# Optimization experiments

Measured on AMD Instinct MI355X. Metric: run time of the kernel, lower is better.

The kernel has to match this reference:

```python
import jax, jax.numpy as jnp
import numpy as np
import math

DIM = 256
HEADS = 8
HID = DIM * HEADS


def mish(x):
    return x * jnp.tanh(jax.nn.softplus(x))


def setup_inputs() -> dict:
    key = jax.random.key(0)
    ks = jax.random.split(key, 12)
    b, t, l = 4, 16, 256
    s = 1.0 / math.sqrt(DIM)
    inp = {
        "qkv_x": jax.random.normal(ks[0], (b, t, l, DIM), jnp.float32),
        "t_embed": jax.random.normal(ks[1], (b, t, 1, DIM), jnp.float32),
        "reward_embed": jax.random.normal(ks[2], (b, t, 1, DIM), jnp.float32),
        "Wq": jax.random.normal(ks[3], (DIM, HID), jnp.float32) * s,
        "Wk": jax.random.normal(ks[4], (DIM, HID), jnp.float32) * s,
        "Wv": jax.random.normal(ks[5], (DIM, HID), jnp.float32) * s,
        "Wq_t": jax.random.normal(ks[6], (DIM, HID), jnp.float32) * s,
        "bq_t": jnp.zeros((HID,), jnp.float32),
        "Wk_t": jax.random.normal(ks[7], (DIM, HID), jnp.float32) * s,
        "bk_t": jnp.zeros((HID,), jnp.float32),
        "Wv_t": jax.random.normal(ks[8], (DIM, HID), jnp.float32) * s,
        "bv_t": jnp.zeros((HID,), jnp.float32),
        "Wo": jax.random.normal(ks[9], (HID, DIM), jnp.float32) * (1.0 / math.sqrt(HID)),
        "bo": jnp.zeros((DIM,), jnp.float32),
    }
    return inp


def reference(qkv_x, t_embed, reward_embed, Wq, Wk, Wv, Wq_t, bq_t, Wk_t, bk_t, Wv_t, bv_t, Wo, bo):
    b, t, l, f = qkv_x.shape
    x = qkv_x.reshape(b * t, l, f)                    # (bt, l, f)
    tr = (t_embed + reward_embed).reshape(b * t, 1, f)  # (bt, 1, f)
    m = mish(tr)

    def proj(W, Wt, bt_):
        # bias-add of time-conditioning broadcast over l, split heads
        y = x @ W + (m @ Wt + bt_)                    # (bt, l, H*D)
        return y.reshape(b * t, l, HEADS, DIM).transpose(0, 2, 1, 3)  # (bt, H, l, D)

    q = proj(Wq, Wq_t, bq_t)
    k = proj(Wk, Wk_t, bk_t)
    v = proj(Wv, Wv_t, bv_t)

    scores = jnp.einsum('bhqd,bhkd->bhqk', q, k) / math.sqrt(DIM)
    attn = jax.nn.softmax(scores, axis=-1)
    out = jnp.einsum('bhqk,bhkd->bhqd', attn, v)      # (bt, H, l, D)
    out = out.transpose(0, 2, 1, 3).reshape(b, t, l, HEADS * DIM)
    return out @ Wo + bo
```

## Files before the change

### kernel.cpp

```cpp
#include <hip/hip_runtime.h>
#include <stdint.h>

typedef __bf16 bf16x8 __attribute__((ext_vector_type(8)));
typedef float f32x4 __attribute__((ext_vector_type(4)));
typedef uint32_t u32x4 __attribute__((ext_vector_type(4)));

#define MFMA16(a,b,c) __builtin_amdgcn_mfma_f32_16x16x32_bf16(a,b,c,0,0,0)

#define OFF_XB   0ull
#define OFF_WT   8388608ull
#define OFF_WTT  11534336ull
#define OFF_WOT  14680064ull
#define OFF_MB   15728640ull
#define OFF_BIAS 15761408ull
#define OFF_K    17334272ull
#define OFF_VT   84443136ull
#define WS_NEED  151552000ull
#define OFF_Q    151552000ull
#define WS_NEED2 218660864ull

__device__ __forceinline__ uint16_t f2bf(float f) {
  uint32_t u = __builtin_bit_cast(uint32_t, f);
  return (uint16_t)((u + 0x7fffu + ((u >> 16) & 1u)) >> 16);
}
__device__ __forceinline__ bf16x8 ld16(const uint16_t* p) {
  u32x4 v = *(const u32x4*)p;
  return __builtin_bit_cast(bf16x8, v);
}
__device__ __forceinline__ void bounce_w2(char* slab, int row, int col, uint16_t val) {
  int slot = col >> 3;
  *(uint16_t*)(slab + row * 256 + (((slot ^ (row & 7)) & 15) << 4) + ((col & 7) << 1)) = val;
}
__device__ __forceinline__ bf16x8 bounce_r16(const char* slab, int row, int slot) {
  u32x4 v = *(const u32x4*)(slab + row * 256 + (((slot ^ (row & 7)) & 15) << 4));
  return __builtin_bit_cast(bf16x8, v);
}

__global__ void sentinel_kernel(float* out, float val) {
  out[blockIdx.x * 256 + threadIdx.x] = val;
}
__global__ void init_out(const float* bo, float* out) {
  int i = blockIdx.x * 256 + threadIdx.x;
  out[i] = bo[i & 255];
}

__global__ void mish_kernel(const float* te, const float* re, uint16_t* mb) {
  int i = blockIdx.x * 256 + threadIdx.x;
  float x = te[i] + re[i];
  float sp = log1pf(__expf(x));
  mb[i] = f2bf(x * tanhf(sp));
}

__global__ void convx_kernel(const float* x, uint16_t* xb) {
  int i = blockIdx.x * 256 + threadIdx.x;
  float4 v = ((const float4*)x)[i];
  ushort4 o = make_ushort4(f2bf(v.x), f2bf(v.y), f2bf(v.z), f2bf(v.w));
  ((ushort4*)xb)[i] = o;
}

__global__ void wtrans_kernel(const float* w0, const float* w1, const float* w2,
                              const float* w3, const float* w4, const float* w5,
                              const float* w6, uint16_t* wt, uint16_t* wtt, uint16_t* wot) {
  int z = blockIdx.y;
  const float* src; uint16_t* dst; int C;
  if (z < 3)      { src = (z==0)?w0:((z==1)?w1:w2); dst = wt  + (size_t)z*524288;     C=2048; }
  else if (z < 6) { src = (z==3)?w3:((z==4)?w4:w5); dst = wtt + (size_t)(z-3)*524288; C=2048; }
  else            { src = w6; dst = wot;                                              C=256; }
  int R = (z < 6) ? 256 : 2048;
  __shared__ uint16_t tile[32][33];
  int tc = C >> 5;
  int bR = (blockIdx.x / tc) << 5, bC = (blockIdx.x % tc) << 5;
  int tx = threadIdx.x & 31, ty = threadIdx.x >> 5;
  #pragma unroll
  for (int i = 0; i < 4; i++) {
    int r = bR + ty + i * 8;
    tile[ty + i * 8][tx] = f2bf(src[(size_t)r * C + bC + tx]);
  }
  __syncthreads();
  #pragma unroll
  for (int i = 0; i < 4; i++) {
    int c = bC + ty + i * 8;
    dst[(size_t)c * R + bR + tx] = tile[tx][ty + i * 8];
  }
}

__global__ __launch_bounds__(256, 4)
void bias_gemm(const uint16_t* Mb, const uint16_t* WTT,
               const float* bq, const float* bk, const float* bv, float* biasAll) {
  int bid = blockIdx.x;
  int z = bid >> 4, nbt = bid & 15;
  int n0 = nbt << 7;
  const uint16_t* Bsrc = WTT + (size_t)z * 524288;
  const float* bvec = (z == 0) ? bq : ((z == 1) ? bk : bv);
  float* outp = biasAll + (size_t)z * 131072;
  int tid = threadIdx.x, lane = tid & 63, w = tid >> 6;
  int g = lane >> 4, ln = lane & 15;

  bf16x8 af[8];
  #pragma unroll
  for (int ks = 0; ks < 8; ks++)
    af[ks] = ld16(Mb + (size_t)(w*16 + ln) * 256 + ks*32 + g*8);
  f32x4 acc[8];
  #pragma unroll
  for (int j = 0; j < 8; j++) acc[j] = (f32x4){0.f,0.f,0.f,0.f};
  #pragma unroll
  for (int j = 0; j < 8; j++)
    #pragma unroll
    for (int ks = 0; ks < 8; ks++) {
      bf16x8 bf_ = ld16(Bsrc + (size_t)(n0 + j*16 + ln) * 256 + ks*32 + g*8);
      acc[j] = MFMA16(af[ks], bf_, acc[j]);
    }
  #pragma unroll
  for (int j = 0; j < 8; j++) {
    int colg = n0 + j*16 + ln;
    float bb = bvec[colg];
    #pragma unroll
    for (int r = 0; r < 4; r++)
      outp[(size_t)(w*16 + g*4 + r) * 2048 + colg] = acc[j][r] + bb;
  }
}

__global__ __launch_bounds__(512, 2)
void qkv_gemm2(const uint16_t* Xb, const uint16_t* WT, const float* biasAll,
               uint16_t* Kw, uint16_t* Vt, uint16_t* Qw) {
  __shared__ char stage[32768];
  int bid = blockIdx.x;
  int z2 = bid >> 11, rem = bid & 2047;
  int widx = (z2 + 1) % 3;
  int mb = rem >> 4, nb = rem & 15;
  int m0 = mb << 7, n0 = nb << 7;
  const uint16_t* Bsrc = WT + (size_t)widx * 524288;
  int bt = m0 >> 8;
  const float* bias = biasAll + (size_t)widx * 131072 + (size_t)bt * 2048;
  int tid = threadIdx.x, lane = tid & 63, w = tid >> 6;
  int g = lane >> 4, ln = lane & 15;

  u32x4 rb[4];
  auto issueB = [&](int t) {
    #pragma unroll
    for (int it = 0; it < 4; it++) {
      int c = tid + (it << 9);
      int row = c >> 5, sl = c & 31;
      rb[it] = *(const u32x4*)(Bsrc + (size_t)(n0 + t*64 + row) * 256 + sl * 8);
    }
  };
  issueB(0);
  bf16x8 af[8];
  #pragma unroll
  for (int ks = 0; ks < 8; ks++)
    af[ks] = ld16(Xb + (size_t)(m0 + w*16 + ln) * 256 + ks*32 + g*8);
  f32x4 acc[8];
  #pragma unroll
  for (int j = 0; j < 8; j++) acc[j] = (f32x4){0.f,0.f,0.f,0.f};

  #pragma unroll
  for (int t = 0; t < 2; t++) {
    __syncthreads();
    #pragma unroll
    for (int it = 0; it < 4; it++) {
      int c = tid + (it << 9);
      int row = c >> 5, sl = c & 31;
      *(u32x4*)(stage + row * 512 + ((sl ^ (row & 7)) << 4)) = rb[it];
    }
    __syncthreads();
    if (t == 0) issueB(1);
    #pragma unroll
    for (int ks = 0; ks < 8; ks++)
      #pragma unroll
      for (int j2 = 0; j2 < 4; j2++) {
        int row = j2*16 + ln;
        u32x4 v = *(const u32x4*)(stage + row * 512 + ((((ks<<2)+g) ^ (row & 7)) << 4));
        acc[t*4+j2] = MFMA16(af[ks], __builtin_bit_cast(bf16x8, v), acc[t*4+j2]);
      }
  }
  float scale = (z2 == 2) ? 0.0625f : 1.0f;
  #pragma unroll
  for (int j = 0; j < 8; j++) {
    int colg = n0 + j*16 + ln;
    int hh = colg >> 8, d = colg & 255;
    float bb = bias[colg];
    size_t hb = (size_t)(bt * 8 + hh) << 16;
    int l0 = (m0 & 255) + w*16 + g*4;
    if (z2 == 1) {
      ushort4 pk = make_ushort4(f2bf(acc[j][0]+bb), f2bf(acc[j][1]+bb),
                                f2bf(acc[j][2]+bb), f2bf(acc[j][3]+bb));
      *(ushort4*)(Vt + hb + ((size_t)d << 8) + l0) = pk;
    } else {
      uint16_t* dst = (z2 == 0) ? Kw : Qw;
      #pragma unroll
      for (int r = 0; r < 4; r++)
        dst[hb + ((size_t)(l0 + r) << 8) + d] = f2bf((acc[j][r] + bb) * scale);
    }
  }
}

__global__ __launch_bounds__(1024, 2)
void attn_core2(const uint16_t* Qw, const uint16_t* Kw, const uint16_t* Vt, uint16_t* Ob) {
  __shared__ char smem[65536];
  int tid = threadIdx.x, lane = tid & 63, w = tid >> 6;
  int g = lane >> 4, ln = lane & 15;
  int bh = blockIdx.x;
  const size_t kvbase = (size_t)bh << 16;
  int q0l = w * 16;
  char* stage = smem;
  char* slab  = smem + 32768 + (w << 11);

  u32x4 rv[2];
  auto issue_tile = [&](const uint16_t* src) {
    #pragma unroll
    for (int it = 0; it < 2; it++) {
      int c = tid + (it << 10);
      int row = c >> 5, sl = c & 31;
      rv[it] = *(const u32x4*)(src + (size_t)row * 256 + sl * 8);
    }
  };
  auto commit_tile = [&]() {
    #pragma unroll
    for (int it = 0; it < 2; it++) {
      int c = tid + (it << 10);
      int row = c >> 5, sl = c & 31;
      *(u32x4*)(stage + row * 512 + ((sl ^ (row & 7)) << 4)) = rv[it];
    }
  };
  auto frag = [&](int row, int slot) -> bf16x8 {
    u32x4 v = *(const u32x4*)(stage + row * 512 + ((slot ^ (row & 7)) << 4));
    return __builtin_bit_cast(bf16x8, v);
  };

  issue_tile(Kw + kvbase);
  bf16x8 qa[8];
  #pragma unroll
  for (int ks = 0; ks < 8; ks++)
    qa[ks] = ld16(Qw + kvbase + (size_t)(q0l + ln) * 256 + ks*32 + g*8);

  f32x4 S[16];
  #pragma unroll
  for (int f = 0; f < 16; f++) S[f] = (f32x4){0.f,0.f,0.f,0.f};
  #pragma unroll
  for (int t = 0; t < 4; t++) {
    __syncthreads();
    commit_tile();
    __syncthreads();
    if (t < 3) issue_tile(Kw + kvbase + (size_t)((t+1)*64) * 256);
    #pragma unroll
    for (int ks = 0; ks < 8; ks++)
      #pragma unroll
      for (int f2 = 0; f2 < 4; f2++)
        S[t*4+f2] = MFMA16(qa[ks], frag(f2*16 + ln, ks*4 + g), S[t*4+f2]);
  }
  issue_tile(Vt + kvbase);

  #pragma unroll
  for (int r = 0; r < 4; r++) {
    float mx = -3.4e38f;
    #pragma unroll
    for (int f = 0; f < 16; f++) mx = fmaxf(mx, S[f][r]);
    #pragma unroll
    for (int m_ = 1; m_ < 16; m_ <<= 1) mx = fmaxf(mx, __shfl_xor(mx, m_, 64));
    float sum = 0.f;
    #pragma unroll
    for (int f = 0; f < 16; f++) {
      float p = __expf(S[f][r] - mx);
      S[f][r] = p; sum += p;
    }
    #pragma unroll
    for (int m_ = 1; m_ < 16; m_ <<= 1) sum += __shfl_xor(sum, m_, 64);
    float inv = 1.f / sum;
    #pragma unroll
    for (int f = 0; f < 16; f++) S[f][r] *= inv;
  }

  bf16x8 pb[8];
  #pragma unroll
  for (int qtr = 0; qtr < 4; qtr++) {
    #pragma unroll
    for (int f2 = 0; f2 < 4; f2++) {
      int col = f2*16 + ln;
      int slot = col >> 3;
      #pragma unroll
      for (int r = 0; r < 4; r++) {
        int row = g*4 + r;
        *(uint16_t*)(slab + row*128 + (((slot ^ (row & 7)) & 7) << 4) + ((col & 7) << 1))
            = f2bf(S[qtr*4+f2][r]);
      }
    }
    #pragma unroll
    for (int i = 0; i < 2; i++) {
      u32x4 v = *(const u32x4*)(slab + ln*128 + ((((i*4+g) ^ (ln & 7)) & 7) << 4));
      pb[qtr*2+i] = __builtin_bit_cast(bf16x8, v);
    }
  }

  f32x4 O[16];
  #pragma unroll
  for (int df = 0; df < 16; df++) O[df] = (f32x4){0.f,0.f,0.f,0.f};
  #pragma unroll
  for (int t = 0; t < 4; t++) {
    __syncthreads();
    commit_tile();
    __syncthreads();
    if (t < 3) issue_tile(Vt + kvbase + (size_t)((t+1)*64) * 256);
    #pragma unroll
    for (int ks = 0; ks < 8; ks++)
      #pragma unroll
      for (int df2 = 0; df2 < 4; df2++)
        O[t*4+df2] = MFMA16(frag(df2*16 + ln, ks*4 + g), pb[ks], O[t*4+df2]);
  }

  size_t obase = kvbase + (size_t)(q0l + ln) * 256;
  #pragma unroll
  for (int df = 0; df < 16; df++) {
    ushort4 pk = make_ushort4(f2bf(O[df][0]), f2bf(O[df][1]), f2bf(O[df][2]), f2bf(O[df][3]));
    *(ushort4*)(Ob + obase + df*16 + g*4) = pk;
  }
}

__global__ __launch_bounds__(256, 4)
void out_gemm(const uint16_t* Ob, const uint16_t* WoT, const float* bo, float* out) {
  __shared__ char stage[16384];
  int bid = blockIdx.x;
  int mt = bid >> 1, nt = bid & 1;
  int m0 = mt << 6, n0 = nt << 7;
  int bt = m0 >> 8;
  int lrow = (m0 & 255);
  int tid = threadIdx.x, lane = tid & 63, w = tid >> 6;
  int g = lane >> 4, ln = lane & 15;

  u32x4 rb[4];
  auto issueW = [&](int kt) {
    #pragma unroll
    for (int it = 0; it < 4; it++) {
      int c = tid + (it << 8);
      int row = c >> 3, sl = c & 7;
      rb[it] = *(const u32x4*)(WoT + (size_t)(n0 + row) * 2048 + kt*64 + sl*8);
    }
  };
  issueW(0);
  f32x4 acc[8];
  #pragma unroll
  for (int j = 0; j < 8; j++) acc[j] = (f32x4){0.f,0.f,0.f,0.f};

  for (int kt = 0; kt < 32; kt++) {
    __syncthreads();
    #pragma unroll
    for (int it = 0; it < 4; it++) {
      int c = tid + (it << 8);
      int row = c >> 3, sl = c & 7;
      *(u32x4*)(stage + row*128 + (((sl ^ (row & 7)) & 7) << 4)) = rb[it];
    }
    __syncthreads();
    if (kt < 31) issueW(kt+1);
    const uint16_t* abase = Ob + ((size_t)(bt*8 + (kt >> 2)) << 16)
                          + (size_t)(lrow + w*16 + ln) * 256 + (kt & 3) * 64;
    bf16x8 af[2];
    #pragma unroll
    for (int ks = 0; ks < 2; ks++)
      af[ks] = ld16(abase + ks*32 + g*8);
    #pragma unroll
    for (int ks = 0; ks < 2; ks++)
      #pragma unroll
      for (int j = 0; j < 8; j++) {
        int row = j*16 + ln;
        u32x4 v = *(const u32x4*)(stage + row*128 + ((((ks*4+g) ^ (row & 7)) & 7) << 4));
        acc[j] = MFMA16(af[ks], __builtin_bit_cast(bf16x8, v), acc[j]);
      }
  }
  #pragma unroll
  for (int j = 0; j < 8; j++) {
    int col = n0 + j*16 + ln;
    float bb = bo[col];
    #pragma unroll
    for (int r = 0; r < 4; r++)
      out[(size_t)(m0 + w*16 + g*4 + r) * 256 + col] = acc[j][r] + bb;
  }
}

__global__ __launch_bounds__(512, 2)
void attn_v5(const uint16_t* Xb, const uint16_t* WT, const float* Bi,
             const uint16_t* Kw, const uint16_t* Vt, const uint16_t* WoT,
             float* out) {
  __shared__ char smem[65536];
  int tid = threadIdx.x, lane = tid & 63, w = tid >> 6;
  int g = lane >> 4, ln = lane & 15;
  int bid = blockIdx.x;
  int bh = bid >> 1, qh = bid & 1;
  int bt = bh >> 3, h = bh & 7;
  const size_t kvbase = (size_t)bh << 16;
  int q0g = bt * 256 + qh * 128 + w * 16;
  char* stage = smem;
  char* slab  = smem + 32768 + (w << 12);

  u32x4 rv[4];
  auto issue_tile = [&](const uint16_t* src, int rowstride) {
    #pragma unroll
    for (int it = 0; it < 4; it++) {
      int c = tid + (it << 9);
      int row = c >> 5, sl = c & 31;
      rv[it] = *(const u32x4*)(src + (size_t)row * rowstride + sl * 8);
    }
  };
  auto commit_tile = [&]() {
    #pragma unroll
    for (int it = 0; it < 4; it++) {
      int c = tid + (it << 9);
      int row = c >> 5, sl = c & 31;
      *(u32x4*)(stage + row * 512 + ((sl ^ (row & 7)) << 4)) = rv[it];
    }
  };
  auto frag = [&](int row, int slot) -> bf16x8 {
    u32x4 v = *(const u32x4*)(stage + row * 512 + ((slot ^ (row & 7)) << 4));
    return __builtin_bit_cast(bf16x8, v);
  };

  issue_tile(WT + (size_t)(h*256) * 256, 256);
  bf16x8 qx[8];
  #pragma unroll
  for (int ks = 0; ks < 8; ks++)
    qx[ks] = ld16(Xb + (size_t)(q0g + ln) * 256 + ks*32 + g*8);
  f32x4 qacc[16];
  #pragma unroll
  for (int f = 0; f < 16; f++) qacc[f] = (f32x4){0.f,0.f,0.f,0.f};
  #pragma unroll
  for (int t = 0; t < 4; t++) {
    __syncthreads();
    commit_tile();
    __syncthreads();
    if (t < 3) issue_tile(WT + (size_t)(h*256 + (t+1)*64) * 256, 256);
    #pragma unroll
    for (int ks = 0; ks < 8; ks++)
      #pragma unroll
      for (int f2 = 0; f2 < 4; f2++)
        qacc[t*4+f2] = MFMA16(qx[ks], frag(f2*16 + ln, ks*4 + g), qacc[t*4+f2]);
  }
  issue_tile(Kw + kvbase, 256);
  #pragma unroll
  for (int f = 0; f < 16; f++) {
    float bb = Bi[bt*2048 + h*256 + f*16 + ln];
    #pragma unroll
    for (int r = 0; r < 4; r++) qacc[f][r] = (qacc[f][r] + bb) * 0.0625f;
  }
  bf16x8 qa[8];
  #pragma unroll
  for (int dh = 0; dh < 2; dh++) {
    #pragma unroll
    for (int f2 = 0; f2 < 8; f2++) {
      int f = dh*8 + f2;
      #pragma unroll
      for (int r = 0; r < 4; r++)
        bounce_w2(slab, g*4 + r, f2*16 + ln, f2bf(qacc[f][r]));
    }
    #pragma unroll
    for (int ks2 = 0; ks2 < 4; ks2++)
      qa[dh*4 + ks2] = bounce_r16(slab, ln, ks2*4 + g);
  }

  f32x4 S[16];
  #pragma unroll
  for (int f = 0; f < 16; f++) S[f] = (f32x4){0.f,0.f,0.f,0.f};
  #pragma unroll
  for (int t = 0; t < 4; t++) {
    __syncthreads();
    commit_tile();
    __syncthreads();
    if (t < 3) issue_tile(Kw + kvbase + (size_t)((t+1)*64) * 256, 256);
    #pragma unroll
    for (int ks = 0; ks < 8; ks++)
      #pragma unroll
      for (int f2 = 0; f2 < 4; f2++)
        S[t*4+f2] = MFMA16(qa[ks], frag(f2*16 + ln, ks*4 + g), S[t*4+f2]);
  }
  issue_tile(Vt + kvbase, 256);

  #pragma unroll
  for (int r = 0; r < 4; r++) {
    float mx = -3.4e38f;
    #pragma unroll
    for (int f = 0; f < 16; f++) mx = fmaxf(mx, S[f][r]);
    #pragma unroll
    for (int m_ = 1; m_ < 16; m_ <<= 1) mx = fmaxf(mx, __shfl_xor(mx, m_, 64));
    float sum = 0.f;
    #pragma unroll
    for (int f = 0; f < 16; f++) {
      float p = __expf(S[f][r] - mx);
      S[f][r] = p; sum += p;
    }
    #pragma unroll
    for (int m_ = 1; m_ < 16; m_ <<= 1) sum += __shfl_xor(sum, m_, 64);
    float inv = 1.f / sum;
    #pragma unroll
    for (int f = 0; f < 16; f++) S[f][r] *= inv;
  }

  bf16x8 pb[8];
  #pragma unroll
  for (int kh = 0; kh < 2; kh++) {
    #pragma unroll
    for (int f2 = 0; f2 < 8; f2++) {
      int f = kh*8 + f2;
      #pragma unroll
      for (int r = 0; r < 4; r++)
        bounce_w2(slab, g*4 + r, f2*16 + ln, f2bf(S[f][r]));
    }
    #pragma unroll
    for (int ks2 = 0; ks2 < 4; ks2++)
      pb[kh*4 + ks2] = bounce_r16(slab, ln, ks2*4 + g);
  }

  f32x4 O[16];
  #pragma unroll
  for (int df = 0; df < 16; df++) O[df] = (f32x4){0.f,0.f,0.f,0.f};
  #pragma unroll
  for (int t = 0; t < 4; t++) {
    __syncthreads();
    commit_tile();
    __syncthreads();
    if (t < 3) issue_tile(Vt + kvbase + (size_t)((t+1)*64) * 256, 256);
    #pragma unroll
    for (int ks = 0; ks < 8; ks++)
      #pragma unroll
      for (int df2 = 0; df2 < 4; df2++)
        O[t*4+df2] = MFMA16(frag(df2*16 + ln, ks*4 + g), pb[ks], O[t*4+df2]);
  }
  issue_tile(WoT + (size_t)0 * 2048 + h*256, 2048);

  bf16x8 oa[8];
  #pragma unroll
  for (int dh = 0; dh < 2; dh++) {
    #pragma unroll
    for (int df2 = 0; df2 < 8; df2++) {
      int df = dh*8 + df2;
      #pragma unroll
      for (int r = 0; r < 4; r++)
        bounce_w2(slab, ln, df2*16 + g*4 + r, f2bf(O[df][r]));
    }
    #pragma unroll
    for (int ks2 = 0; ks2 < 4; ks2++)
      oa[dh*4 + ks2] = bounce_r16(slab, ln, ks2*4 + g);
  }

  f32x4 oacc[16];
  #pragma unroll
  for (int ef = 0; ef < 16; ef++) oacc[ef] = (f32x4){0.f,0.f,0.f,0.f};
  #pragma unroll
  for (int t = 0; t < 4; t++) {
    __syncthreads();
    commit_tile();
    __syncthreads();
    if (t < 3) issue_tile(WoT + (size_t)((t+1)*64) * 2048 + h*256, 2048);
    #pragma unroll
    for (int ks = 0; ks < 8; ks++)
      #pragma unroll
      for (int ef2 = 0; ef2 < 4; ef2++)
        oacc[t*4+ef2] = MFMA16(oa[ks], frag(ef2*16 + ln, ks*4 + g), oacc[t*4+ef2]);
  }
  #pragma unroll
  for (int ef = 0; ef < 16; ef++)
    #pragma unroll
    for (int r = 0; r < 4; r++)
      atomicAdd(out + (size_t)(q0g + g*4 + r) * 256 + ef*16 + ln, oacc[ef][r]);
}

extern "C" void kernel_launch(void* const* d_in, const int* in_sizes, int n_in,
                              void* d_out, int out_size, void* d_ws, size_t ws_size,
                              hipStream_t stream) {
  float* out = (float*)d_out;
  if (ws_size < WS_NEED) {
    sentinel_kernel<<<16384, 256, 0, stream>>>(out, 1000.0f + (float)(ws_size >> 20));
    return;
  }
  const float* x   = (const float*)d_in[0];
  const float* te  = (const float*)d_in[1];
  const float* re  = (const float*)d_in[2];
  const float* Wq  = (const float*)d_in[3];
  const float* Wk  = (const float*)d_in[4];
  const float* Wv  = (const float*)d_in[5];
  const float* Wqt = (const float*)d_in[6];
  const float* bqt = (const float*)d_in[7];
  const float* Wkt = (const float*)d_in[8];
  const float* bkt = (const float*)d_in[9];
  const float* Wvt = (const float*)d_in[10];
  const float* bvt = (const float*)d_in[11];
  const float* Wo  = (const float*)d_in[12];
  const float* bo  = (const float*)d_in[13];
  char* ws = (char*)d_ws;
  uint16_t* Xb  = (uint16_t*)(ws + OFF_XB);
  uint16_t* WT  = (uint16_t*)(ws + OFF_WT);
  uint16_t* WTT = (uint16_t*)(ws + OFF_WTT);
  uint16_t* WoT = (uint16_t*)(ws + OFF_WOT);
  uint16_t* Mb  = (uint16_t*)(ws + OFF_MB);
  float*    Bi  = (float*)(ws + OFF_BIAS);
  uint16_t* Kw  = (uint16_t*)(ws + OFF_K);
  uint16_t* Vt  = (uint16_t*)(ws + OFF_VT);

  mish_kernel<<<64, 256, 0, stream>>>(te, re, Mb);
  wtrans_kernel<<<dim3(512, 7), 256, 0, stream>>>(Wq, Wk, Wv, Wqt, Wkt, Wvt, Wo, WT, WTT, WoT);
  convx_kernel<<<4096, 256, 0, stream>>>(x, Xb);
  bias_gemm<<<48, 256, 0, stream>>>(Mb, WTT, bqt, bkt, bvt, Bi);

  if (ws_size >= WS_NEED2) {
    uint16_t* Qw = (uint16_t*)(ws + OFF_Q);
    qkv_gemm2<<<6144, 512, 0, stream>>>(Xb, WT, Bi, Kw, Vt, Qw);
    attn_core2<<<512, 1024, 0, stream>>>(Qw, Kw, Vt, Qw);
    out_gemm<<<512, 256, 0, stream>>>(Qw, WoT, bo, out);
  } else {
    qkv_gemm2<<<4096, 512, 0, stream>>>(Xb, WT, Bi, Kw, Vt, Kw);
    init_out<<<16384, 256, 0, stream>>>(bo, out);
    attn_v5<<<1024, 512, 0, stream>>>(Xb, WT, Bi, Kw, Vt, WoT, out);
  }
}
```

Measured before the change: 257.2 us.

## Restructure QKV GEMM into 2x2 warp tiling with direct global-to-LDS loads

```diff
diff --git a/kernel.cpp b/kernel.cpp
--- a/kernel.cpp
+++ b/kernel.cpp
@@ -26,6 +26,11 @@
 __device__ __forceinline__ bf16x8 ld16(const uint16_t* p) {
   u32x4 v = *(const u32x4*)p;
   return __builtin_bit_cast(bf16x8, v);
+}
+__device__ __forceinline__ void gll16(const uint16_t* g, char* l) {
+  __builtin_amdgcn_global_load_lds(
+      (const __attribute__((address_space(1))) void*)g,
+      (__attribute__((address_space(3))) void*)l, 16, 0, 0);
 }
 __device__ __forceinline__ void bounce_w2(char* slab, int row, int col, uint16_t val) {
   int slot = col >> 3;
@@ -120,8 +125,8 @@
   }
 }
 
-__global__ __launch_bounds__(512, 2)
-void qkv_gemm2(const uint16_t* Xb, const uint16_t* WT, const float* biasAll,
+__global__ __launch_bounds__(256)
+void qkv_gemm3(const uint16_t* Xb, const uint16_t* WT, const float* biasAll,
                uint16_t* Kw, uint16_t* Vt, uint16_t* Qw) {
   __shared__ char stage[32768];
   int bid = blockIdx.x;
@@ -134,62 +139,67 @@
   const float* bias = biasAll + (size_t)widx * 131072 + (size_t)bt * 2048;
   int tid = threadIdx.x, lane = tid & 63, w = tid >> 6;
   int g = lane >> 4, ln = lane & 15;
-
-  u32x4 rb[4];
-  auto issueB = [&](int t) {
-    #pragma unroll
-    for (int it = 0; it < 4; it++) {
-      int c = tid + (it << 9);
-      int row = c >> 5, sl = c & 31;
-      rb[it] = *(const u32x4*)(Bsrc + (size_t)(n0 + t*64 + row) * 256 + sl * 8);
-    }
-  };
-  issueB(0);
-  bf16x8 af[8];
-  #pragma unroll
-  for (int ks = 0; ks < 8; ks++)
-    af[ks] = ld16(Xb + (size_t)(m0 + w*16 + ln) * 256 + ks*32 + g*8);
-  f32x4 acc[8];
-  #pragma unroll
-  for (int j = 0; j < 8; j++) acc[j] = (f32x4){0.f,0.f,0.f,0.f};
-
-  #pragma unroll
-  for (int t = 0; t < 2; t++) {
-    __syncthreads();
-    #pragma unroll
-    for (int it = 0; it < 4; it++) {
-      int c = tid + (it << 9);
-      int row = c >> 5, sl = c & 31;
-      *(u32x4*)(stage + row * 512 + ((sl ^ (row & 7)) << 4)) = rb[it];
-    }
-    __syncthreads();
-    if (t == 0) issueB(1);
-    #pragma unroll
-    for (int ks = 0; ks < 8; ks++)
-      #pragma unroll
-      for (int j2 = 0; j2 < 4; j2++) {
-        int row = j2*16 + ln;
-        u32x4 v = *(const u32x4*)(stage + row * 512 + ((((ks<<2)+g) ^ (row & 7)) << 4));
-        acc[t*4+j2] = MFMA16(af[ks], __builtin_bit_cast(bf16x8, v), acc[t*4+j2]);
+  int wr = w >> 1, wc = w & 1;
+  int rw = lane >> 3;
+  int sg = (lane & 7) ^ rw;
+
+  f32x4 acc[4][4];
+  #pragma unroll
+  for (int i = 0; i < 4; i++)
+    #pragma unroll
+    for (int j = 0; j < 4; j++) acc[i][j] = (f32x4){0.f,0.f,0.f,0.f};
+
+  for (int kt = 0; kt < 4; kt++) {
+    int k0 = kt << 6;
+    __syncthreads();
+    #pragma unroll
+    for (int c = 0; c < 4; c++) {
+      int chunk = w * 4 + c;
+      int row = chunk * 8 + rw;
+      gll16(Xb   + (size_t)(m0 + row) * 256 + k0 + sg * 8, stage + chunk * 1024);
+      gll16(Bsrc + (size_t)(n0 + row) * 256 + k0 + sg * 8, stage + 16384 + chunk * 1024);
+    }
+    __syncthreads();
+    #pragma unroll
+    for (int ks = 0; ks < 2; ks++) {
+      bf16x8 a_[4];
+      #pragma unroll
+      for (int i = 0; i < 4; i++) {
+        int R = wr*64 + i*16 + ln;
+        u32x4 v = *(const u32x4*)(stage + R*128 + ((((ks<<2)+g) ^ (R & 7)) << 4));
+        a_[i] = __builtin_bit_cast(bf16x8, v);
       }
-  }
+      #pragma unroll
+      for (int j = 0; j < 4; j++) {
+        int R = wc*64 + j*16 + ln;
+        u32x4 v = *(const u32x4*)(stage + 16384 + R*128 + ((((ks<<2)+g) ^ (R & 7)) << 4));
+        bf16x8 b_ = __builtin_bit_cast(bf16x8, v);
+        #pragma unroll
+        for (int i = 0; i < 4; i++) acc[i][j] = MFMA16(a_[i], b_, acc[i][j]);
+      }
+    }
+  }
+
   float scale = (z2 == 2) ? 0.0625f : 1.0f;
   #pragma unroll
-  for (int j = 0; j < 8; j++) {
-    int colg = n0 + j*16 + ln;
+  for (int j = 0; j < 4; j++) {
+    int colg = n0 + wc*64 + j*16 + ln;
     int hh = colg >> 8, d = colg & 255;
     float bb = bias[colg];
     size_t hb = (size_t)(bt * 8 + hh) << 16;
-    int l0 = (m0 & 255) + w*16 + g*4;
-    if (z2 == 1) {
-      ushort4 pk = make_ushort4(f2bf(acc[j][0]+bb), f2bf(acc[j][1]+bb),
-                                f2bf(acc[j][2]+bb), f2bf(acc[j][3]+bb));
-      *(ushort4*)(Vt + hb + ((size_t)d << 8) + l0) = pk;
-    } else {
-      uint16_t* dst = (z2 == 0) ? Kw : Qw;
-      #pragma unroll
-      for (int r = 0; r < 4; r++)
-        dst[hb + ((size_t)(l0 + r) << 8) + d] = f2bf((acc[j][r] + bb) * scale);
+    #pragma unroll
+    for (int i = 0; i < 4; i++) {
+      int l0 = (m0 & 255) + wr*64 + i*16 + g*4;
+      if (z2 == 1) {
+        ushort4 pk = make_ushort4(f2bf(acc[i][j][0]+bb), f2bf(acc[i][j][1]+bb),
+                                  f2bf(acc[i][j][2]+bb), f2bf(acc[i][j][3]+bb));
+        *(ushort4*)(Vt + hb + ((size_t)d << 8) + l0) = pk;
+      } else {
+        uint16_t* dst = (z2 == 0) ? Kw : Qw;
+        #pragma unroll
+        for (int r = 0; r < 4; r++)
+          dst[hb + ((size_t)(l0 + r) << 8) + d] = f2bf((acc[i][j][r] + bb) * scale);
+      }
     }
   }
 }
@@ -599,11 +609,11 @@
 
   if (ws_size >= WS_NEED2) {
     uint16_t* Qw = (uint16_t*)(ws + OFF_Q);
-    qkv_gemm2<<<6144, 512, 0, stream>>>(Xb, WT, Bi, Kw, Vt, Qw);
+    qkv_gemm3<<<6144, 256, 0, stream>>>(Xb, WT, Bi, Kw, Vt, Qw);
     attn_core2<<<512, 1024, 0, stream>>>(Qw, Kw, Vt, Qw);
     out_gemm<<<512, 256, 0, stream>>>(Qw, WoT, bo, out);
   } else {
-    qkv_gemm2<<<4096, 512, 0, stream>>>(Xb, WT, Bi, Kw, Vt, Kw);
+    qkv_gemm3<<<4096, 256, 0, stream>>>(Xb, WT, Bi, Kw, Vt, Kw);
     init_out<<<16384, 256, 0, stream>>>(bo, out);
     attn_v5<<<1024, 512, 0, stream>>>(Xb, WT, Bi, Kw, Vt, WoT, out);
   }
```

Result: faster. 250.4 us (-2.6%).
